# Kernel tuning notes

Measured on AMD Instinct MI355X. Metric: run time of the kernel, lower is better.

Reference implementation:

```python
import jax, jax.numpy as jnp
import numpy as np

GAMMA = 0.1
B, C, H, W = 8, 64, 64, 64
CINT = C // 8


def setup_inputs() -> dict:
    key = jax.random.key(0)
    ks = jax.random.split(key, 5)
    x = jax.random.normal(ks[0], (B, C, H, W), dtype=jnp.float32)
    Wq = jax.random.normal(ks[1], (CINT, C), dtype=jnp.float32) * 0.05
    Wk = jax.random.normal(ks[2], (CINT, C), dtype=jnp.float32) * 0.05
    Wv = jax.random.normal(ks[3], (CINT, C), dtype=jnp.float32) * 0.05
    Wout = jax.random.normal(ks[4], (C, CINT), dtype=jnp.float32) * 0.05
    return {"x": x, "Wq": Wq, "Wk": Wk, "Wv": Wv, "Wout": Wout}


def reference(x, Wq, Wk, Wv, Wout):
    b, c, h, w = x.shape
    n = h * w
    cint = Wq.shape[0]
    xf = x.reshape(b, c, n)                               # [B,C,N]
    q = jnp.einsum('ic,bcn->bin', Wq, xf)                 # [B,Cint,N]
    k = jnp.einsum('ic,bcn->bin', Wk, xf)
    v = jnp.einsum('ic,bcn->bin', Wv, xf)
    # scores[b, n, m] = q[b,:,n] . k[b,:,m]; softmax over dim=1 (the n axis)
    scores = jnp.einsum('bin,bim->bnm', q, k) / jnp.sqrt(jnp.asarray(cint, x.dtype))
    att = jax.nn.softmax(scores, axis=1)                  # [B,N,N], softmax over rows
    att_out = jnp.einsum('bin,bnm->bim', v, att)          # [B,Cint,N]
    out = jnp.einsum('ci,bim->bcm', Wout, att_out)        # [B,C,N]
    return x + out.reshape(b, c, h, w) * GAMMA
```

## Files before the change

kernel.cpp:

```cpp
#include <hip/hip_runtime.h>
#include <math.h>

#define BB 8
#define CC 64
#define NN 4096
#define CI 8
#define GAMMA 0.1f
#define SCALE (1.44269504088896f * 0.35355339059327f)
#define NSPLIT 8

typedef float v4f  __attribute__((ext_vector_type(4)));
typedef float v16f __attribute__((ext_vector_type(16)));
typedef __bf16 bf16x8 __attribute__((ext_vector_type(8)));
typedef __bf16 bf16x4 __attribute__((ext_vector_type(4)));

__device__ __forceinline__ float fast_exp2(float x) {
    return __builtin_amdgcn_exp2f(x);
}

__global__ __launch_bounds__(256) void qkv_kernel(
        const float* __restrict__ x,
        const float* __restrict__ Wq, const float* __restrict__ Wk,
        const float* __restrict__ Wv,
        __bf16* __restrict__ qbh, __bf16* __restrict__ kbh,
        __bf16* __restrict__ vbh, float* __restrict__ attab) {
    __shared__ float sw[3 * CI * CC];
    __shared__ unsigned short sq[32 * 8];
    __shared__ unsigned short sk[32 * 8];
    const int t = threadIdx.x;
    const int i  = t >> 5;
    const int nl = t & 31;
    const int b  = blockIdx.y;
    const int n0 = blockIdx.x * 32;

    for (int idx = t; idx < CI * CC; idx += 256) {
        sw[idx]                = Wq[idx];
        sw[CI * CC + idx]      = Wk[idx] * SCALE;
        sw[2 * CI * CC + idx]  = Wv[idx];
    }
    int lin = (blockIdx.y * (NN / 32) + blockIdx.x) * 256 + t;
    for (int idx = lin; idx < BB * 9 * NN; idx += BB * NN * CI) attab[idx] = 0.f;
    __syncthreads();

    const int n = n0 + nl;
    const float* xp = x + ((size_t)b * CC) * NN + n;
    const v4f* wq4 = (const v4f*)(sw + i * CC);
    const v4f* wk4 = (const v4f*)(sw + CI * CC + i * CC);
    const v4f* wv4 = (const v4f*)(sw + 2 * CI * CC + i * CC);
    float qa = 0.f, ka = 0.f, va = 0.f;
#pragma unroll 4
    for (int c4 = 0; c4 < CC / 4; ++c4) {
        v4f wq = wq4[c4], wk = wk4[c4], wv = wv4[c4];
        float x0 = xp[(size_t)(c4 * 4 + 0) * NN];
        float x1 = xp[(size_t)(c4 * 4 + 1) * NN];
        float x2 = xp[(size_t)(c4 * 4 + 2) * NN];
        float x3 = xp[(size_t)(c4 * 4 + 3) * NN];
        qa = fmaf(wq.x, x0, qa); ka = fmaf(wk.x, x0, ka); va = fmaf(wv.x, x0, va);
        qa = fmaf(wq.y, x1, qa); ka = fmaf(wk.y, x1, ka); va = fmaf(wv.y, x1, va);
        qa = fmaf(wq.z, x2, qa); ka = fmaf(wk.z, x2, ka); va = fmaf(wv.z, x2, va);
        qa = fmaf(wq.w, x3, qa); ka = fmaf(wk.w, x3, ka); va = fmaf(wv.w, x3, va);
    }
    __bf16 vb = (__bf16)va;
    vbh[((size_t)b * CI + i) * NN + n] = vb;
    __bf16 qb = (__bf16)qa, kb2 = (__bf16)ka;
    sq[nl * 8 + i] = *(unsigned short*)&qb;
    sk[nl * 8 + i] = *(unsigned short*)&kb2;
    __syncthreads();
    if (t < 32) {
        *(uint4*)(qbh + ((size_t)b * NN + n0 + t) * 8) = *(const uint4*)(sq + t * 8);
        *(uint4*)(kbh + ((size_t)b * NN + n0 + t) * 8) = *(const uint4*)(sk + t * 8);
    }
}

__global__ __launch_bounds__(256) void att_kernel(
        const __bf16* __restrict__ qbh, const __bf16* __restrict__ kbh,
        const __bf16* __restrict__ vbh, float* __restrict__ attab) {
    __shared__ unsigned short eld[4][32 * 36];
    const int t = threadIdx.x;
    const int w    = t >> 6;
    const int l    = t & 63;
    const int ln   = l & 31;
    const int hi   = l >> 5;
    const int quad = l >> 4;
    const int lm   = l & 15;
    const int b  = blockIdx.z;
    const int m0 = blockIdx.x * 128 + w * 32;
    const int nbase = blockIdx.y * (NN / NSPLIT);
    const int NCH = (NN / NSPLIT) / 32;

    bf16x8 zero8, ones8;
#pragma unroll
    for (int z = 0; z < 8; ++z) { zero8[z] = (__bf16)0.0f; ones8[z] = (__bf16)1.0f; }

    bf16x8 kfragB = hi ? zero8
                       : *(const bf16x8*)(kbh + ((size_t)b * NN + m0 + ln) * 8);

    const __bf16* qrow = qbh + (size_t)b * NN * 8;
    const __bf16* vrow = vbh + ((size_t)b * CI + (lm & 7)) * NN;
    const bool v_v = (lm < 8);
    const bool v_1 = (lm == 8);

    unsigned short* tile = eld[w];
    unsigned short* wr   = tile + ln * 36 + hi * 4;
    const unsigned short* rd0 = tile + lm * 36 + quad * 8;
    const unsigned short* rd1 = tile + (16 + lm) * 36 + quad * 8;

    v4f acc0 = {0.f, 0.f, 0.f, 0.f};
    v4f acc1 = {0.f, 0.f, 0.f, 0.f};

    for (int ch = 0; ch < NCH; ++ch) {
        const int nc = nbase + ch * 32;
        bf16x8 qfrag = hi ? zero8
                          : *(const bf16x8*)(qrow + (size_t)(nc + ln) * 8);
        bf16x8 vfrag = v_v ? *(const bf16x8*)(vrow + nc + quad * 8)
                           : (v_1 ? ones8 : zero8);

        v16f S = __builtin_amdgcn_mfma_f32_32x32x16_bf16(
            qfrag, kfragB,
            (v16f){0.f,0.f,0.f,0.f,0.f,0.f,0.f,0.f,0.f,0.f,0.f,0.f,0.f,0.f,0.f,0.f},
            0, 0, 0);

#pragma unroll
        for (int g = 0; g < 4; ++g) {
            bf16x4 e;
            e[0] = (__bf16)fast_exp2(S[4 * g + 0]);
            e[1] = (__bf16)fast_exp2(S[4 * g + 1]);
            e[2] = (__bf16)fast_exp2(S[4 * g + 2]);
            e[3] = (__bf16)fast_exp2(S[4 * g + 3]);
            *(bf16x4*)(wr + g * 8) = e;
        }

        bf16x8 ef0 = *(const bf16x8*)(rd0);
        bf16x8 ef1 = *(const bf16x8*)(rd1);
        acc0 = __builtin_amdgcn_mfma_f32_16x16x32_bf16(vfrag, ef0, acc0, 0, 0, 0);
        acc1 = __builtin_amdgcn_mfma_f32_16x16x32_bf16(vfrag, ef1, acc1, 0, 0, 0);
    }

    float* ap = attab + (size_t)b * 9 * NN + m0;
    float a0[4] = {acc0.x, acc0.y, acc0.z, acc0.w};
    float a1[4] = {acc1.x, acc1.y, acc1.z, acc1.w};
#pragma unroll
    for (int r = 0; r < 4; ++r) {
        int i = quad * 4 + r;
        if (i < 9) {
            atomicAdd(ap + (size_t)i * NN + lm, a0[r]);
            atomicAdd(ap + (size_t)i * NN + 16 + lm, a1[r]);
        }
    }
}

__global__ __launch_bounds__(256) void out_kernel(
        const float* __restrict__ x, const float* __restrict__ Wout,
        const float* __restrict__ attab, float* __restrict__ out) {
    const int t = threadIdx.x;
    const int c = blockIdx.y;
    const int b = blockIdx.z;
    const int m = (blockIdx.x * 256 + t) * 4;
    const float* ap = attab + (size_t)b * 9 * NN + m;
    v4f sum = *(const v4f*)(ap + (size_t)8 * NN);
    v4f s = {0.f, 0.f, 0.f, 0.f};
#pragma unroll
    for (int i = 0; i < CI; ++i) {
        float wgt = Wout[c * CI + i];
        v4f a = *(const v4f*)(ap + (size_t)i * NN);
        s.x = fmaf(wgt, a.x, s.x);
        s.y = fmaf(wgt, a.y, s.y);
        s.z = fmaf(wgt, a.z, s.z);
        s.w = fmaf(wgt, a.w, s.w);
    }
    size_t o = ((size_t)b * CC + c) * NN + m;
    v4f xv = *(const v4f*)(x + o);
    v4f r;
    r.x = xv.x + GAMMA * (s.x / sum.x);
    r.y = xv.y + GAMMA * (s.y / sum.y);
    r.z = xv.z + GAMMA * (s.z / sum.z);
    r.w = xv.w + GAMMA * (s.w / sum.w);
    *(v4f*)(out + o) = r;
}

extern "C" void kernel_launch(void* const* d_in, const int* in_sizes, int n_in,
                              void* d_out, int out_size, void* d_ws, size_t ws_size,
                              hipStream_t stream) {
    const float* x    = (const float*)d_in[0];
    const float* Wq   = (const float*)d_in[1];
    const float* Wk   = (const float*)d_in[2];
    const float* Wv   = (const float*)d_in[3];
    const float* Wout = (const float*)d_in[4];
    float* out = (float*)d_out;

    __bf16* qbh = (__bf16*)d_ws;
    __bf16* kbh = qbh + (size_t)BB * NN * 8;
    __bf16* vbh = kbh + (size_t)BB * NN * 8;
    float* attab = (float*)(vbh + (size_t)BB * NN * 8);

    qkv_kernel<<<dim3(NN / 32, BB), 256, 0, stream>>>(x, Wq, Wk, Wv, qbh, kbh, vbh, attab);
    att_kernel<<<dim3(NN / 128, NSPLIT, BB), 256, 0, stream>>>(qbh, kbh, vbh, attab);
    out_kernel<<<dim3(NN / 1024, CC, BB), 256, 0, stream>>>(x, Wout, attab, out);
}
```

Measured before the change: 113.3 us.

## Keep exp scores in registers via permlane32 swap instead of LDS transpose

The attention kernel no longer stages the exponentiated score tile through shared memory to re-layout it as the second MFMA operand. It packs pairs of exp values with v_cvt_pk_bf16_f32, exchanges halves across the two 32-lane groups with permlane32_swap, and feeds them directly into two 32x32x16 MFMAs accumulating a single 16-wide accumulator. This removes LDS writes and reads, and any associated waits, from the inner loop, at the cost of wasting more MFMA rows (only 9 of 32 used) and issuing extra V loads per chunk.

```diff
diff --git a/kernel.cpp b/kernel.cpp
--- a/kernel.cpp
+++ b/kernel.cpp
@@ -13,9 +13,16 @@
 typedef float v16f __attribute__((ext_vector_type(16)));
 typedef __bf16 bf16x8 __attribute__((ext_vector_type(8)));
 typedef __bf16 bf16x4 __attribute__((ext_vector_type(4)));
+typedef unsigned int u32x2 __attribute__((ext_vector_type(2)));
 
 __device__ __forceinline__ float fast_exp2(float x) {
     return __builtin_amdgcn_exp2f(x);
+}
+
+__device__ __forceinline__ unsigned int cvt_pk_bf16(float lo, float hi) {
+    unsigned int r;
+    asm("v_cvt_pk_bf16_f32 %0, %1, %2" : "=v"(r) : "v"(lo), "v"(hi));
+    return r;
 }
 
 __global__ __launch_bounds__(256) void qkv_kernel(
@@ -75,14 +82,11 @@
 __global__ __launch_bounds__(256) void att_kernel(
         const __bf16* __restrict__ qbh, const __bf16* __restrict__ kbh,
         const __bf16* __restrict__ vbh, float* __restrict__ attab) {
-    __shared__ unsigned short eld[4][32 * 36];
     const int t = threadIdx.x;
     const int w    = t >> 6;
     const int l    = t & 63;
     const int ln   = l & 31;
     const int hi   = l >> 5;
-    const int quad = l >> 4;
-    const int lm   = l & 15;
     const int b  = blockIdx.z;
     const int m0 = blockIdx.x * 128 + w * 32;
     const int nbase = blockIdx.y * (NN / NSPLIT);
@@ -96,56 +100,53 @@
                        : *(const bf16x8*)(kbh + ((size_t)b * NN + m0 + ln) * 8);
 
     const __bf16* qrow = qbh + (size_t)b * NN * 8;
-    const __bf16* vrow = vbh + ((size_t)b * CI + (lm & 7)) * NN;
-    const bool v_v = (lm < 8);
-    const bool v_1 = (lm == 8);
-
-    unsigned short* tile = eld[w];
-    unsigned short* wr   = tile + ln * 36 + hi * 4;
-    const unsigned short* rd0 = tile + lm * 36 + quad * 8;
-    const unsigned short* rd1 = tile + (16 + lm) * 36 + quad * 8;
-
-    v4f acc0 = {0.f, 0.f, 0.f, 0.f};
-    v4f acc1 = {0.f, 0.f, 0.f, 0.f};
+    const __bf16* vrow = vbh + ((size_t)b * CI + (ln & 7)) * NN;
+    const bool v_live = (ln < 8);
+    const bool v_ones = (ln == 8);
+
+    v16f acc = {0.f,0.f,0.f,0.f,0.f,0.f,0.f,0.f,0.f,0.f,0.f,0.f,0.f,0.f,0.f,0.f};
 
     for (int ch = 0; ch < NCH; ++ch) {
         const int nc = nbase + ch * 32;
         bf16x8 qfrag = hi ? zero8
                           : *(const bf16x8*)(qrow + (size_t)(nc + ln) * 8);
-        bf16x8 vfrag = v_v ? *(const bf16x8*)(vrow + nc + quad * 8)
-                           : (v_1 ? ones8 : zero8);
+        bf16x8 va0 = v_live ? *(const bf16x8*)(vrow + nc + hi * 8)
+                            : (v_ones ? ones8 : zero8);
+        bf16x8 va1 = v_live ? *(const bf16x8*)(vrow + nc + 16 + hi * 8)
+                            : (v_ones ? ones8 : zero8);
 
         v16f S = __builtin_amdgcn_mfma_f32_32x32x16_bf16(
             qfrag, kfragB,
             (v16f){0.f,0.f,0.f,0.f,0.f,0.f,0.f,0.f,0.f,0.f,0.f,0.f,0.f,0.f,0.f,0.f},
             0, 0, 0);
 
+        unsigned int pk0 = cvt_pk_bf16(fast_exp2(S[0]),  fast_exp2(S[1]));
+        unsigned int pk1 = cvt_pk_bf16(fast_exp2(S[2]),  fast_exp2(S[3]));
+        unsigned int pk2 = cvt_pk_bf16(fast_exp2(S[4]),  fast_exp2(S[5]));
+        unsigned int pk3 = cvt_pk_bf16(fast_exp2(S[6]),  fast_exp2(S[7]));
+        unsigned int pk4 = cvt_pk_bf16(fast_exp2(S[8]),  fast_exp2(S[9]));
+        unsigned int pk5 = cvt_pk_bf16(fast_exp2(S[10]), fast_exp2(S[11]));
+        unsigned int pk6 = cvt_pk_bf16(fast_exp2(S[12]), fast_exp2(S[13]));
+        unsigned int pk7 = cvt_pk_bf16(fast_exp2(S[14]), fast_exp2(S[15]));
+
+        u32x2 r02 = __builtin_amdgcn_permlane32_swap(pk0, pk2, false, false);
+        u32x2 r13 = __builtin_amdgcn_permlane32_swap(pk1, pk3, false, false);
+        u32x2 r46 = __builtin_amdgcn_permlane32_swap(pk4, pk6, false, false);
+        u32x2 r57 = __builtin_amdgcn_permlane32_swap(pk5, pk7, false, false);
+
+        union { unsigned int u[4]; bf16x8 f; } e0f, e1f;
+        e0f.u[0] = r02[0]; e0f.u[1] = r13[0]; e0f.u[2] = r02[1]; e0f.u[3] = r13[1];
+        e1f.u[0] = r46[0]; e1f.u[1] = r57[0]; e1f.u[2] = r46[1]; e1f.u[3] = r57[1];
+
+        acc = __builtin_amdgcn_mfma_f32_32x32x16_bf16(va0, e0f.f, acc, 0, 0, 0);
+        acc = __builtin_amdgcn_mfma_f32_32x32x16_bf16(va1, e1f.f, acc, 0, 0, 0);
+    }
+
+    float* ap = attab + (size_t)b * 9 * NN + m0 + ln;
 #pragma unroll
-        for (int g = 0; g < 4; ++g) {
-            bf16x4 e;
-            e[0] = (__bf16)fast_exp2(S[4 * g + 0]);
-            e[1] = (__bf16)fast_exp2(S[4 * g + 1]);
-            e[2] = (__bf16)fast_exp2(S[4 * g + 2]);
-            e[3] = (__bf16)fast_exp2(S[4 * g + 3]);
-            *(bf16x4*)(wr + g * 8) = e;
-        }
-
-        bf16x8 ef0 = *(const bf16x8*)(rd0);
-        bf16x8 ef1 = *(const bf16x8*)(rd1);
-        acc0 = __builtin_amdgcn_mfma_f32_16x16x32_bf16(vfrag, ef0, acc0, 0, 0, 0);
-        acc1 = __builtin_amdgcn_mfma_f32_16x16x32_bf16(vfrag, ef1, acc1, 0, 0, 0);
-    }
-
-    float* ap = attab + (size_t)b * 9 * NN + m0;
-    float a0[4] = {acc0.x, acc0.y, acc0.z, acc0.w};
-    float a1[4] = {acc1.x, acc1.y, acc1.z, acc1.w};
-#pragma unroll
-    for (int r = 0; r < 4; ++r) {
-        int i = quad * 4 + r;
-        if (i < 9) {
-            atomicAdd(ap + (size_t)i * NN + lm, a0[r]);
-            atomicAdd(ap + (size_t)i * NN + 16 + lm, a1[r]);
-        }
+    for (int r = 0; r < 16; ++r) {
+        int io = (r & 3) + 8 * (r >> 2) + 4 * hi;
+        if (io < 9) atomicAdd(ap + (size_t)io * NN, acc[r]);
     }
 }
 
```

Measured after the change: 108.3 us. 1.05x faster.
